# Optimization experiments

Hardware: AMD Instinct MI355X
Metric: run time of the kernel (lower is better)

Reference implementation:

```python
import jax, jax.numpy as jnp
import numpy as np

NINP = 1024
NHID = 1024
STEPS = 8
INITRANGE = 0.04
T, B = 256, 64

# DARTS_V1 recurrent genotype: (activation, predecessor-state index)
GENOTYPE = [("sigmoid", 0), ("relu", 1), ("relu", 1), ("identity", 1),
            ("tanh", 2), ("sigmoid", 5), ("tanh", 3), ("relu", 5)]

ACT = {
    "tanh": jnp.tanh,
    "relu": jax.nn.relu,
    "sigmoid": jax.nn.sigmoid,
    "identity": lambda x: x,
    "selu": jax.nn.selu,
}


def setup_inputs() -> dict:
    key = jax.random.key(0)
    k_in, k_w0, k_ws = jax.random.split(key, 3)
    inputs = jax.random.normal(k_in, (T, B, NINP), dtype=jnp.float32)
    hidden = jnp.zeros((1, B, NHID), dtype=jnp.float32)
    W0 = jax.random.uniform(k_w0, (NINP + NHID, 2 * NHID),
                            minval=-INITRANGE, maxval=INITRANGE, dtype=jnp.float32)
    Ws = jax.random.uniform(k_ws, (STEPS, NHID, 2 * NHID),
                            minval=-INITRANGE, maxval=INITRANGE, dtype=jnp.float32)
    return {"inputs": inputs, "hidden": hidden, "W0": W0, "Ws": Ws}


def _cell(x, h_prev, W0, Ws):
    # init state: highway combine of gated candidate with previous hidden
    xh = jnp.concatenate([x, h_prev], axis=-1)            # [B, ninp+nhid]
    c0, h0 = jnp.split(xh @ W0, 2, axis=-1)               # [B, nhid] each
    s0 = h_prev + jax.nn.sigmoid(c0) * (jnp.tanh(h0) - h_prev)
    states = [s0]
    for i, (name, pred) in enumerate(GENOTYPE):
        s_prev = states[pred]
        c, h = jnp.split(s_prev @ Ws[i], 2, axis=-1)      # [B, nhid] each
        s = s_prev + jax.nn.sigmoid(c) * (ACT[name](h) - s_prev)
        states.append(s)
    # output = mean over the DAG intermediate states (concat = range(1, steps+1))
    return jnp.mean(jnp.stack(states[1:], axis=0), axis=0)


def reference(inputs, hidden, W0, Ws):
    h0 = hidden[0]                                        # [B, nhid]

    def step(h, x_t):
        h_new = _cell(x_t, h, W0, Ws)
        return h_new, h_new

    _, hiddens = jax.lax.scan(step, h0, inputs)           # [T, B, nhid]
    return hiddens
```

## Files before the change

### kernel.cpp

```cpp
#include <hip/hip_runtime.h>
#include <math.h>


typedef __attribute__((ext_vector_type(8))) _Float16 half8;
typedef __attribute__((ext_vector_type(4))) float f32x4;
typedef __attribute__((ext_vector_type(8))) unsigned short us8;

#define NH 1024
#define SCALE 2048.f
#define INVS  (1.f/2048.f)
#define WF_BYTES 83886080ull
#define FA_BYTES 1572864ull
#define T_STEPS  256

#define LBAR() asm volatile("s_waitcnt lgkmcnt(0)\n\ts_barrier" ::: "memory")

__device__ __forceinline__ float sigf(float x){ return 1.f/(1.f+__expf(-x)); }
__device__ __forceinline__ void limbs2(float x, _Float16& a, _Float16& b){
    a = (_Float16)x; b = (_Float16)((x - (float)a)*SCALE);
}

struct Pre { const float* W0; const float* Ws; unsigned short* wf; };

__global__ __launch_bounds__(256) void preconv(Pre d) {
    int gid  = blockIdx.x * 4 + (threadIdx.x >> 6);
    int lane = threadIdx.x & 63;
    const float* W; unsigned short* dst; int nks, cg, ks;
    if (gid < 8192) {
        W = d.W0; dst = d.wf; nks = 64; cg = gid >> 6; ks = gid & 63;
    } else {
        int g = gid - 8192; int mm = g >> 12; int wi = g & 4095;
        W   = d.Ws + (size_t)mm * (1024 * 2048);
        dst = d.wf + 8388608ull + (size_t)mm * 4194304ull;
        nks = 32; cg = wi >> 5; ks = wi & 31;
    }
    int c  = cg * 16 + (lane & 15);
    int kb = ks * 32 + (lane >> 4) * 8;
    half8 h0, h1;
    #pragma unroll
    for (int j = 0; j < 8; ++j) {
        _Float16 p, q; limbs2(W[(size_t)(kb + j) * 2048 + c], p, q);
        h0[j] = p; h1[j] = q;
    }
    unsigned short* o = dst + ((size_t)cg * nks + ks) * 1024 + lane * 8;
    *(half8*)o         = h0;
    *(half8*)(o + 512) = h1;
}

__global__ __launch_bounds__(256) void initk(const float* hidden, char* fa, unsigned* flags) {
    int gid = blockIdx.x * 256 + threadIdx.x;
    if (gid < 1536) flags[gid] = (gid < 256) ? 1u : 0u;
    #pragma unroll
    for (int e = 0; e < 4; ++e) {
        int i = gid * 4 + e;
        int row = i >> 10, col = i & 1023;
        int rt = row >> 4, rowf = row & 15;
        int ksp = col >> 5, kin = col & 31;
        int lanep = (kin >> 3) * 16 + rowf;
        size_t off = (size_t)rt * 65536 + ((size_t)ksp * 64 + lanep) * 32 + (kin & 7) * 4;
        _Float16 u0, u1; limbs2(hidden[i], u0, u1);
        unsigned pk = (unsigned)__builtin_bit_cast(unsigned short, u0) |
                      ((unsigned)__builtin_bit_cast(unsigned short, u1) << 16);
        *(unsigned*)(fa + off) = pk;
    }
}

__device__ __forceinline__ void aload(const char* fa, int ks, int lane, half8& a0, half8& a1) {
    const char* p = fa + ((size_t)ks * 64 + lane) * 32;
    us8 q0 = *(const us8*)p;
    us8 q1 = *(const us8*)(p + 16);
    a0 = __builtin_bit_cast(half8, __builtin_shufflevector(q0, q1, 0,2,4,6,8,10,12,14));
    a1 = __builtin_bit_cast(half8, __builtin_shufflevector(q0, q1, 1,3,5,7,9,11,13,15));
}
__device__ __forceinline__ half8 ldw(const unsigned short* p) { return *(const half8*)p; }
__device__ __forceinline__ void mfma6(half8 a0, half8 a1, half8 w0, half8 w1,
                                      f32x4& x0, f32x4& x1) {
    x0 = __builtin_amdgcn_mfma_f32_16x16x32_f16(a0, w0, x0, 0, 0, 0);
    x1 = __builtin_amdgcn_mfma_f32_16x16x32_f16(a0, w1, x1, 0, 0, 0);
    x1 = __builtin_amdgcn_mfma_f32_16x16x32_f16(a1, w0, x1, 0, 0, 0);
}
__device__ __forceinline__ void rwrite1(float* arena, int wave, int lane,
        f32x4 c0, f32x4 c1, f32x4 h0, f32x4 h1) {
    float* b = arena + wave * 512;
    #pragma unroll
    for (int r = 0; r < 4; ++r) {
        b[lane * 4 + r]       = c0[r] + c1[r] * INVS;
        b[256 + lane * 4 + r] = h0[r] + h1[r] * INVS;
    }
}
__device__ __forceinline__ void rsum1(const float* arena, int idx, float& cs, float& hs) {
    float c = 0.f, h = 0.f;
    #pragma unroll
    for (int w = 0; w < 16; ++w) {
        c += arena[w * 512 + idx];
        h += arena[w * 512 + 256 + idx];
    }
    cs = c; hs = h;
}
__device__ __forceinline__ void fstore(char* fa, int offp, float v) {
    _Float16 u0, u1; limbs2(v, u0, u1);
    unsigned pk = (unsigned)__builtin_bit_cast(unsigned short, u0) |
                  ((unsigned)__builtin_bit_cast(unsigned short, u1) << 16);
    __hip_atomic_store((unsigned*)(fa + offp), pk, __ATOMIC_RELAXED, __HIP_MEMORY_SCOPE_AGENT);
}
template<int ACQ>
__device__ __forceinline__ void pollw(unsigned* f, unsigned tgt, int lane) {
    unsigned v = __hip_atomic_load(f + lane, __ATOMIC_RELAXED, __HIP_MEMORY_SCOPE_AGENT);
    while (__ballot(v < tgt)) {
        __builtin_amdgcn_s_sleep(2);
        v = __hip_atomic_load(f + lane, __ATOMIC_RELAXED, __HIP_MEMORY_SCOPE_AGENT);
    }
    if (ACQ)
        (void)__hip_atomic_load(f, __ATOMIC_ACQUIRE, __HIP_MEMORY_SCOPE_AGENT);
}
__device__ __forceinline__ void publish(unsigned* slot, unsigned v) {
    __hip_atomic_store(slot, v, __ATOMIC_RELAXED, __HIP_MEMORY_SCOPE_AGENT);
}

struct PK {
    const float* x; const float* hidden;
    const unsigned short* wf;
    char* fa; unsigned* flags; float* out;
};

__global__ __launch_bounds__(1024) void persist(PK p) {
    __shared__ float arena[16 * 512];

    const int tid = threadIdx.x;
    const int wave = tid >> 6, lane = tid & 63;
    const int l15 = lane & 15, lg = lane >> 4;
    const int lane8 = lane * 8, lg8 = lg * 8;
    const int bx = blockIdx.x;
    const int cg = (bx & 7) * 8 + ((bx >> 3) & 7);
    const int rt = bx >> 6;

    const unsigned short* wf0 = p.wf;
    const unsigned short* wfs[8];
    #pragma unroll
    for (int i = 0; i < 8; ++i) wfs[i] = p.wf + 8388608ull + (size_t)i * 4194304ull;

    char* FAH  = p.fa + (size_t)(0 * 4 + rt) * 65536;
    char* FAS0 = p.fa + (size_t)(1 * 4 + rt) * 65536;
    char* FAS1 = p.fa + (size_t)(2 * 4 + rt) * 65536;
    char* FAS2 = p.fa + (size_t)(3 * 4 + rt) * 65536;
    char* FAS3 = p.fa + (size_t)(4 * 4 + rt) * 65536;
    char* FAS5 = p.fa + (size_t)(5 * 4 + rt) * 65536;
    #define FLG(tn) (p.flags + ((tn) * 4 + rt) * 64)

    #define WLOAD(wbuf, wfp, nks, kbase) do { \
        _Pragma("unroll") \
        for (int _i = 0; _i < 2; ++_i) { \
            const int _ks = (kbase) + wave * 2 + _i; \
            const unsigned short* _pc = (wfp) + ((size_t)cg * (nks) + _ks) * 1024 + lane8; \
            const unsigned short* _ph = (wfp) + ((size_t)(cg + 64) * (nks) + _ks) * 1024 + lane8; \
            wbuf[_i][0] = ldw(_pc); wbuf[_i][1] = ldw(_pc + 512); \
            wbuf[_i][2] = ldw(_ph); wbuf[_i][3] = ldw(_ph + 512); } } while (0)
    #define ALD(dst0, dst1, fa) do { \
        _Pragma("unroll") \
        for (int _i = 0; _i < 2; ++_i) aload(fa, wave * 2 + _i, lane, dst0[_i], dst1[_i]); } while (0)
    #define GEMM(wbuf, A0, A1, X0, X1, Y0, Y1) do { \
        _Pragma("unroll") \
        for (int _i = 0; _i < 2; ++_i) { \
            mfma6(A0[_i], A1[_i], wbuf[_i][0], wbuf[_i][1], X0, X1); \
            mfma6(A0[_i], A1[_i], wbuf[_i][2], wbuf[_i][3], Y0, Y1); } } while (0)

    const int rowf = tid >> 4, colf = tid & 15;
    const size_t opos = (size_t)(rt * 16 + rowf) * NH + cg * 16 + colf;
    const int idx = colf * 4 + (rowf >> 2) * 64 + (rowf & 3);
    int offp;
    {
        int col = cg * 16 + colf;
        int ksp = col >> 5, kin = col & 31;
        int lanep = (kin >> 3) * 16 + rowf;
        offp = (ksp * 64 + lanep) * 32 + (kin & 7) * 4;
    }
    float hprev = 0.f, s0v = 0.f, s1v = 0.f, s2v = 0.f, s3v = 0.f, s5v = 0.f, runsum = 0.f;
    if (tid < 256) hprev = p.hidden[opos];
    const int xrow = rt * 16 + l15;
    __syncthreads();

    for (int t = 0; t < T_STEPS; ++t) {
        const float* xt = p.x + (size_t)t * 65536;
        half8 a0[2], a1[2];

        f32x4 c0 = {}, c1 = {}, h0 = {}, h1 = {};
        {
            half8 wx[2][4], xa0[2], xa1[2];
            WLOAD(wx, wf0, 64, 0);
            #pragma unroll
            for (int i = 0; i < 2; ++i) {
                const int ks = wave * 2 + i;
                const float* xp = xt + (size_t)xrow * NH + ks * 32 + lg8;
                float4 v0 = *(const float4*)xp, v1 = *(const float4*)(xp + 4);
                float fv[8] = {v0.x, v0.y, v0.z, v0.w, v1.x, v1.y, v1.z, v1.w};
                #pragma unroll
                for (int j = 0; j < 8; ++j) { _Float16 u, w2; limbs2(fv[j], u, w2); xa0[i][j] = u; xa1[i][j] = w2; }
            }
            GEMM(wx, xa0, xa1, c0, c1, h0, h1);
            half8 wh[2][4];
            WLOAD(wh, wf0, 64, 32);
            if (wave == 15) pollw<1>(FLG(0), t + 1, lane);
            __syncthreads();
            half8 ha0[2], ha1[2];
            ALD(ha0, ha1, FAH);
            GEMM(wh, ha0, ha1, c0, c1, h0, h1);
            rwrite1(arena, wave, lane, c0, c1, h0, h1);
        }
        LBAR();
        if (tid < 256) {
            float cs, hs; rsum1(arena, idx, cs, hs);
            s0v = hprev + sigf(cs) * (tanhf(hs) - hprev);
            fstore(FAS0, offp, s0v);
        }
        __syncthreads();
        if (tid == 0) publish(FLG(1) + cg, t + 1);

        {
            half8 w0[2][4];
            WLOAD(w0, wfs[0], 32, 0);
            if (wave == 15) pollw<0>(FLG(1), t + 1, lane);
            __syncthreads();
            ALD(a0, a1, FAS0);
            f32x4 X0 = {}, X1 = {}, Y0 = {}, Y1 = {};
            GEMM(w0, a0, a1, X0, X1, Y0, Y1);
            rwrite1(arena, wave, lane, X0, X1, Y0, Y1);
        }
        LBAR();
        if (tid < 256) {
            float cs, hs; rsum1(arena, idx, cs, hs);
            s1v = s0v + sigf(cs) * (sigf(hs) - s0v);
            fstore(FAS1, offp, s1v);
            runsum = s1v;
        }
        __syncthreads();
        if (tid == 0) publish(FLG(2) + cg, t + 1);

        {
            half8 w1[2][4], w2[2][4];
            WLOAD(w1, wfs[1], 32, 0);
            WLOAD(w2, wfs[2], 32, 0);
            if (wave == 15) pollw<0>(FLG(2), t + 1, lane);
            __syncthreads();
            ALD(a0, a1, FAS1);
            f32x4 X0 = {}, X1 = {}, Y0 = {}, Y1 = {};
            GEMM(w1, a0, a1, X0, X1, Y0, Y1);
            half8 w3[2][4];
            WLOAD(w3, wfs[3], 32, 0);
            rwrite1(arena, wave, lane, X0, X1, Y0, Y1);
            LBAR();
            if (tid < 256) {
                float cs, hs; rsum1(arena, idx, cs, hs);
                s2v = s1v + sigf(cs) * (fmaxf(hs, 0.f) - s1v);
                fstore(FAS2, offp, s2v);
            }
            __syncthreads();
            if (tid == 0) publish(FLG(3) + cg, t + 1);
            X0 = (f32x4){}; X1 = (f32x4){}; Y0 = (f32x4){}; Y1 = (f32x4){};
            GEMM(w2, a0, a1, X0, X1, Y0, Y1);
            rwrite1(arena, wave, lane, X0, X1, Y0, Y1);
            LBAR();
            if (tid < 256) {
                float cs, hs; rsum1(arena, idx, cs, hs);
                s3v = s1v + sigf(cs) * (fmaxf(hs, 0.f) - s1v);
                fstore(FAS3, offp, s3v);
            }
            __syncthreads();
            if (tid == 0) publish(FLG(4) + cg, t + 1);
            X0 = (f32x4){}; X1 = (f32x4){}; Y0 = (f32x4){}; Y1 = (f32x4){};
            GEMM(w3, a0, a1, X0, X1, Y0, Y1);
            rwrite1(arena, wave, lane, X0, X1, Y0, Y1);
            LBAR();
            if (tid < 256) {
                float cs, hs; rsum1(arena, idx, cs, hs);
                float s4v = s1v + sigf(cs) * (hs - s1v);
                runsum += s2v + s3v + s4v;
            }
        }

        {
            half8 w4[2][4], w6[2][4];
            WLOAD(w4, wfs[4], 32, 0);
            WLOAD(w6, wfs[6], 32, 0);
            if (wave == 15) { pollw<0>(FLG(3), t + 1, lane); pollw<0>(FLG(4), t + 1, lane); }
            __syncthreads();
            half8 b0[2], b1[2];
            ALD(a0, a1, FAS2);
            ALD(b0, b1, FAS3);
            f32x4 X0 = {}, X1 = {}, Y0 = {}, Y1 = {};
            GEMM(w4, a0, a1, X0, X1, Y0, Y1);
            f32x4 U0 = {}, U1 = {}, V0 = {}, V1 = {};
            GEMM(w6, b0, b1, U0, U1, V0, V1);
            rwrite1(arena, wave, lane, X0, X1, Y0, Y1);
            LBAR();
            if (tid < 256) {
                float cs, hs; rsum1(arena, idx, cs, hs);
                s5v = s2v + sigf(cs) * (tanhf(hs) - s2v);
                fstore(FAS5, offp, s5v);
            }
            __syncthreads();
            if (tid == 0) publish(FLG(5) + cg, t + 1);
            rwrite1(arena, wave, lane, U0, U1, V0, V1);
            LBAR();
            if (tid < 256) {
                float cs, hs; rsum1(arena, idx, cs, hs);
                float s7v = s3v + sigf(cs) * (tanhf(hs) - s3v);
                runsum += s5v + s7v;
            }
        }

        {
            half8 w5[2][4], w7[2][4];
            WLOAD(w5, wfs[5], 32, 0);
            WLOAD(w7, wfs[7], 32, 0);
            if (wave == 15) pollw<0>(FLG(5), t + 1, lane);
            __syncthreads();
            ALD(a0, a1, FAS5);
            f32x4 X0 = {}, X1 = {}, Y0 = {}, Y1 = {};
            GEMM(w5, a0, a1, X0, X1, Y0, Y1);
            f32x4 U0 = {}, U1 = {}, V0 = {}, V1 = {};
            GEMM(w7, a0, a1, U0, U1, V0, V1);
            rwrite1(arena, wave, lane, X0, X1, Y0, Y1);
            LBAR();
            float c6 = 0.f, h6 = 0.f;
            if (tid < 256) rsum1(arena, idx, c6, h6);
            LBAR();
            rwrite1(arena, wave, lane, U0, U1, V0, V1);
            LBAR();
            if (tid < 256) {
                float c8, h8; rsum1(arena, idx, c8, h8);
                float s6 = s5v + sigf(c6) * (sigf(h6) - s5v);
                float s8 = s5v + sigf(c8) * (fmaxf(h8, 0.f) - s5v);
                float v = 0.125f * (runsum + s6 + s8);
                p.out[(size_t)t * 65536 + opos] = v;
                fstore(FAH, offp, v);
                hprev = v;
            }
            __syncthreads();
            if (tid == 0) publish(FLG(0) + cg, t + 2);
        }
    }
    #undef FLG
    #undef WLOAD
    #undef ALD
    #undef GEMM
}

extern "C" void kernel_launch(void* const* d_in, const int* in_sizes, int n_in,
                              void* d_out, int out_size, void* d_ws, size_t ws_size,
                              hipStream_t stream) {
    (void)in_sizes; (void)n_in; (void)out_size; (void)ws_size;
    const float* inputs = (const float*)d_in[0];
    const float* hidden = (const float*)d_in[1];
    const float* W0     = (const float*)d_in[2];
    const float* Ws     = (const float*)d_in[3];
    float* out = (float*)d_out;

    char* base = (char*)d_ws;
    unsigned short* wf = (unsigned short*)base;
    char* fa = base + WF_BYTES;
    unsigned* flags = (unsigned*)(fa + FA_BYTES);

    initk<<<64, 256, 0, stream>>>(hidden, fa, flags);
    preconv<<<10240, 256, 0, stream>>>(Pre{W0, Ws, wf});

    PK pk{inputs, hidden, wf, fa, flags, out};
    void* args[] = {&pk};
    if (hipLaunchCooperativeKernel((void*)persist, dim3(256), dim3(1024), args, 0, stream) != hipSuccess)
        persist<<<256, 1024, 0, stream>>>(pk);
}
```

Before: 10.22 ms.

## Poll flags in every wave, use nontemporal weight loads, pad reduction arena

```diff
diff --git a/kernel.cpp b/kernel.cpp
--- a/kernel.cpp
+++ b/kernel.cpp
@@ -12,6 +12,7 @@
 #define WF_BYTES 83886080ull
 #define FA_BYTES 1572864ull
 #define T_STEPS  256
+#define AST 516
 
 #define LBAR() asm volatile("s_waitcnt lgkmcnt(0)\n\ts_barrier" ::: "memory")
 
@@ -72,7 +73,14 @@
     a0 = __builtin_bit_cast(half8, __builtin_shufflevector(q0, q1, 0,2,4,6,8,10,12,14));
     a1 = __builtin_bit_cast(half8, __builtin_shufflevector(q0, q1, 1,3,5,7,9,11,13,15));
 }
-__device__ __forceinline__ half8 ldw(const unsigned short* p) { return *(const half8*)p; }
+template<int NT>
+__device__ __forceinline__ half8 ldw(const unsigned short* p) {
+    if constexpr (NT) {
+        us8 v = __builtin_nontemporal_load((const us8*)p);
+        return __builtin_bit_cast(half8, v);
+    }
+    return *(const half8*)p;
+}
 __device__ __forceinline__ void mfma6(half8 a0, half8 a1, half8 w0, half8 w1,
                                       f32x4& x0, f32x4& x1) {
     x0 = __builtin_amdgcn_mfma_f32_16x16x32_f16(a0, w0, x0, 0, 0, 0);
@@ -81,7 +89,7 @@
 }
 __device__ __forceinline__ void rwrite1(float* arena, int wave, int lane,
         f32x4 c0, f32x4 c1, f32x4 h0, f32x4 h1) {
-    float* b = arena + wave * 512;
+    float* b = arena + wave * AST;
     #pragma unroll
     for (int r = 0; r < 4; ++r) {
         b[lane * 4 + r]       = c0[r] + c1[r] * INVS;
@@ -92,8 +100,8 @@
     float c = 0.f, h = 0.f;
     #pragma unroll
     for (int w = 0; w < 16; ++w) {
-        c += arena[w * 512 + idx];
-        h += arena[w * 512 + 256 + idx];
+        c += arena[w * AST + idx];
+        h += arena[w * AST + 256 + idx];
     }
     cs = c; hs = h;
 }
@@ -107,7 +115,7 @@
 __device__ __forceinline__ void pollw(unsigned* f, unsigned tgt, int lane) {
     unsigned v = __hip_atomic_load(f + lane, __ATOMIC_RELAXED, __HIP_MEMORY_SCOPE_AGENT);
     while (__ballot(v < tgt)) {
-        __builtin_amdgcn_s_sleep(2);
+        __builtin_amdgcn_s_sleep(4);
         v = __hip_atomic_load(f + lane, __ATOMIC_RELAXED, __HIP_MEMORY_SCOPE_AGENT);
     }
     if (ACQ)
@@ -124,7 +132,7 @@
 };
 
 __global__ __launch_bounds__(1024) void persist(PK p) {
-    __shared__ float arena[16 * 512];
+    __shared__ float arena[16 * AST];
 
     const int tid = threadIdx.x;
     const int wave = tid >> 6, lane = tid & 63;
@@ -147,14 +155,14 @@
     char* FAS5 = p.fa + (size_t)(5 * 4 + rt) * 65536;
     #define FLG(tn) (p.flags + ((tn) * 4 + rt) * 64)
 
-    #define WLOAD(wbuf, wfp, nks, kbase) do { \
+    #define WLOAD(wbuf, wfp, nks, kbase, NT) do { \
         _Pragma("unroll") \
         for (int _i = 0; _i < 2; ++_i) { \
             const int _ks = (kbase) + wave * 2 + _i; \
             const unsigned short* _pc = (wfp) + ((size_t)cg * (nks) + _ks) * 1024 + lane8; \
             const unsigned short* _ph = (wfp) + ((size_t)(cg + 64) * (nks) + _ks) * 1024 + lane8; \
-            wbuf[_i][0] = ldw(_pc); wbuf[_i][1] = ldw(_pc + 512); \
-            wbuf[_i][2] = ldw(_ph); wbuf[_i][3] = ldw(_ph + 512); } } while (0)
+            wbuf[_i][0] = ldw<NT>(_pc); wbuf[_i][1] = ldw<NT>(_pc + 512); \
+            wbuf[_i][2] = ldw<NT>(_ph); wbuf[_i][3] = ldw<NT>(_ph + 512); } } while (0)
     #define ALD(dst0, dst1, fa) do { \
         _Pragma("unroll") \
         for (int _i = 0; _i < 2; ++_i) aload(fa, wave * 2 + _i, lane, dst0[_i], dst1[_i]); } while (0)
@@ -186,7 +194,7 @@
         f32x4 c0 = {}, c1 = {}, h0 = {}, h1 = {};
         {
             half8 wx[2][4], xa0[2], xa1[2];
-            WLOAD(wx, wf0, 64, 0);
+            WLOAD(wx, wf0, 64, 0, 1);
             #pragma unroll
             for (int i = 0; i < 2; ++i) {
                 const int ks = wave * 2 + i;
@@ -198,7 +206,7 @@
             }
             GEMM(wx, xa0, xa1, c0, c1, h0, h1);
             half8 wh[2][4];
-            WLOAD(wh, wf0, 64, 32);
+            WLOAD(wh, wf0, 64, 32, 1);
             if (wave == 15) pollw<1>(FLG(0), t + 1, lane);
             __syncthreads();
             half8 ha0[2], ha1[2];
@@ -217,9 +225,8 @@
 
         {
             half8 w0[2][4];
-            WLOAD(w0, wfs[0], 32, 0);
-            if (wave == 15) pollw<0>(FLG(1), t + 1, lane);
-            __syncthreads();
+            WLOAD(w0, wfs[0], 32, 0, 0);
+            pollw<0>(FLG(1), t + 1, lane);
             ALD(a0, a1, FAS0);
             f32x4 X0 = {}, X1 = {}, Y0 = {}, Y1 = {};
             GEMM(w0, a0, a1, X0, X1, Y0, Y1);
@@ -237,15 +244,14 @@
 
         {
             half8 w1[2][4], w2[2][4];
-            WLOAD(w1, wfs[1], 32, 0);
-            WLOAD(w2, wfs[2], 32, 0);
-            if (wave == 15) pollw<0>(FLG(2), t + 1, lane);
-            __syncthreads();
+            WLOAD(w1, wfs[1], 32, 0, 0);
+            WLOAD(w2, wfs[2], 32, 0, 0);
+            pollw<0>(FLG(2), t + 1, lane);
             ALD(a0, a1, FAS1);
             f32x4 X0 = {}, X1 = {}, Y0 = {}, Y1 = {};
             GEMM(w1, a0, a1, X0, X1, Y0, Y1);
             half8 w3[2][4];
-            WLOAD(w3, wfs[3], 32, 0);
+            WLOAD(w3, wfs[3], 32, 0, 1);
             rwrite1(arena, wave, lane, X0, X1, Y0, Y1);
             LBAR();
             if (tid < 256) {
@@ -275,14 +281,15 @@
                 float s4v = s1v + sigf(cs) * (hs - s1v);
                 runsum += s2v + s3v + s4v;
             }
+            LBAR();
         }
 
         {
             half8 w4[2][4], w6[2][4];
-            WLOAD(w4, wfs[4], 32, 0);
-            WLOAD(w6, wfs[6], 32, 0);
-            if (wave == 15) { pollw<0>(FLG(3), t + 1, lane); pollw<0>(FLG(4), t + 1, lane); }
-            __syncthreads();
+            WLOAD(w4, wfs[4], 32, 0, 1);
+            WLOAD(w6, wfs[6], 32, 0, 1);
+            pollw<0>(FLG(3), t + 1, lane);
+            pollw<0>(FLG(4), t + 1, lane);
             half8 b0[2], b1[2];
             ALD(a0, a1, FAS2);
             ALD(b0, b1, FAS3);
@@ -306,14 +313,14 @@
                 float s7v = s3v + sigf(cs) * (tanhf(hs) - s3v);
                 runsum += s5v + s7v;
             }
+            LBAR();
         }
 
         {
             half8 w5[2][4], w7[2][4];
-            WLOAD(w5, wfs[5], 32, 0);
-            WLOAD(w7, wfs[7], 32, 0);
-            if (wave == 15) pollw<0>(FLG(5), t + 1, lane);
-            __syncthreads();
+            WLOAD(w5, wfs[5], 32, 0, 1);
+            WLOAD(w7, wfs[7], 32, 0, 1);
+            pollw<0>(FLG(5), t + 1, lane);
             ALD(a0, a1, FAS5);
             f32x4 X0 = {}, X1 = {}, Y0 = {}, Y1 = {};
             GEMM(w5, a0, a1, X0, X1, Y0, Y1);
```

Result: slower. 13.12 ms (+28.4%).
